# Kernel tuning notes

Measured on AMD Instinct MI355X. Metric: run time of the kernel, lower is better.

The kernel has to match this reference:

```python
import jax, jax.numpy as jnp
import numpy as np

BS, SL, D, NH = 2, 2048, 1024, 16
HD = D // NH
SCALE = D ** (-0.5)  # NOTE: source scales by full model dim, not head dim


def setup_inputs() -> dict:
    key = jax.random.key(0)
    k1, k2, k3 = jax.random.split(key, 3)
    return {
        "input_sequence": jax.random.normal(k1, (BS, SL, D), dtype=jnp.float32),
        "w_qkv": jax.random.normal(k2, (D, 3 * D), dtype=jnp.float32) * (D ** -0.5),
        "w_out": jax.random.normal(k3, (D, D), dtype=jnp.float32) * (D ** -0.5),
    }


def reference(input_sequence, w_qkv, w_out):
    bs, sl, od = input_sequence.shape
    nh, hd = NH, od // NH
    qkv = input_sequence @ w_qkv                      # [bs, sl, 3d]
    q, k, v = jnp.split(qkv, 3, axis=-1)              # each [bs, sl, d]
    q = q * SCALE

    def heads(x):  # [bs, sl, d] -> [bs, nh, sl, hd]
        return x.reshape(bs, sl, nh, hd).transpose(0, 2, 1, 3)

    q, k, v = heads(q), heads(k), heads(v)
    scores = jnp.einsum("bhqd,bhkd->bhqk", q, k)      # [bs, nh, sl, sl]
    weights = jax.nn.softmax(scores, axis=-1)
    ctx = jnp.einsum("bhqk,bhkd->bhqd", weights, v)   # [bs, nh, sl, hd]
    ctx = ctx.transpose(0, 2, 1, 3).reshape(bs, sl, od)
    return ctx @ w_out
```

## Files before the change

kernel.cpp:

```cpp
#include <hip/hip_runtime.h>
#include <cstdint>
#include <cstddef>

typedef float f32x4 __attribute__((ext_vector_type(4)));
typedef float f32x16 __attribute__((ext_vector_type(16)));
typedef __bf16 bf16x8 __attribute__((ext_vector_type(8)));
typedef __bf16 bf16x4 __attribute__((ext_vector_type(4)));
typedef uint32_t u32x4 __attribute__((ext_vector_type(4)));

static constexpr int BSZ = 2, SL = 2048, DM = 1024, NH = 16, HD = 64;
static constexpr int MROWS = BSZ * SL;
static constexpr float LOG2E = 1.4426950408889634f;
static constexpr float QSCALE = 0.03125f * LOG2E;

__device__ __forceinline__ f32x4 mfma16(bf16x8 a, bf16x8 b, f32x4 c) {
    return __builtin_amdgcn_mfma_f32_16x16x32_bf16(a, b, c, 0, 0, 0);
}
__device__ __forceinline__ f32x16 mfma32(bf16x8 a, bf16x8 b, f32x16 c) {
    return __builtin_amdgcn_mfma_f32_32x32x16_bf16(a, b, c, 0, 0, 0);
}
__device__ __forceinline__ uint32_t pkbf(float lo, float hi) {
    uint16_t a = __builtin_bit_cast(uint16_t, (__bf16)lo);
    uint16_t b = __builtin_bit_cast(uint16_t, (__bf16)hi);
    return ((uint32_t)b << 16) | (uint32_t)a;
}
__device__ __forceinline__ float fexp2(float x) {
#if __has_builtin(__builtin_amdgcn_exp2f)
    return __builtin_amdgcn_exp2f(x);
#else
    float r; asm volatile("v_exp_f32 %0, %1" : "=v"(r) : "v"(x)); return r;
#endif
}
__device__ __forceinline__ void gload16(const void* g, void* l) {
    __builtin_amdgcn_global_load_lds(
        (const __attribute__((address_space(1))) uint32_t*)g,
        (__attribute__((address_space(3))) uint32_t*)l, 16, 0, 0);
}

__global__ __launch_bounds__(256) void r19_cast(const float* __restrict__ in,
                                                __bf16* __restrict__ out, int n) {
    int i = (blockIdx.x * 256 + threadIdx.x) * 4;
    if (i >= n) return;
    float4 v = *(const float4*)&in[i];
    bf16x4 o;
    o.x = (__bf16)v.x; o.y = (__bf16)v.y; o.z = (__bf16)v.z; o.w = (__bf16)v.w;
    *(bf16x4*)&out[i] = o;
}

__global__ __launch_bounds__(256) void r19_transpose_cast(const float* __restrict__ in,
                                                          __bf16* __restrict__ out,
                                                          int R, int C) {
    __shared__ float tile[32][33];
    int c0 = blockIdx.x * 32, r0 = blockIdx.y * 32;
    int tx = threadIdx.x & 31, ty = threadIdx.x >> 5;
#pragma unroll
    for (int i = 0; i < 32; i += 8)
        tile[ty + i][tx] = in[(size_t)(r0 + ty + i) * C + c0 + tx];
    __syncthreads();
#pragma unroll
    for (int i = 0; i < 32; i += 8)
        out[(size_t)(c0 + ty + i) * R + r0 + tx] = (__bf16)tile[tx][ty + i];
}

__global__ __launch_bounds__(512, 1) void r19_gemm1(
    const __bf16* __restrict__ A, const __bf16* __restrict__ Bt,
    int M, int N, int K,
    __bf16* __restrict__ qb, __bf16* __restrict__ kb, __bf16* __restrict__ vtb)
{
    __shared__ __bf16 arena[65536];
    const int L  = blockIdx.x + 12 * blockIdx.y;
    const int Ls = (L & 7) * 24 + (L >> 3);
    const int bx = Ls % 12, by = Ls / 12;
    const int n0 = bx * 256, m0 = by * 256;

    const int tid  = threadIdx.x;
    const int wave = tid >> 6, lane = tid & 63;
    const int wr = wave >> 2, wc = wave & 3;
    const int lcol = lane & 15, lgrp = lane >> 4;

    const int srow = wave * 16 + (lane >> 3);
    const int slin = lane & 7;

    f32x4 acc[8][4] = {};
    const int NT = K / 64;

#pragma unroll
    for (int q = 0; q < 4; ++q) {
#pragma unroll
        for (int j = 0; j < 2; ++j) {
            const int r = srow + j * 8;
            const int slot = slin ^ (r & 7);
            const __bf16* src = (q < 2)
                ? &A [(size_t)(m0 + q * 128 + r) * K + slot * 8]
                : &Bt[(size_t)(n0 + (q - 2) * 128 + r) * K + slot * 8];
            gload16(src, &arena[(q < 2 ? q * 8192 : 16384 + (q - 2) * 8192)
                                + (wave * 2 + j) * 512]);
        }
    }
    asm volatile("s_waitcnt vmcnt(0)" ::: "memory");
    __builtin_amdgcn_s_barrier();
    __builtin_amdgcn_sched_barrier(0);

    for (int t = 0; t < NT; ++t) {
        const int cur = t & 1;
        const __bf16* Ab = &arena[cur * 32768];
        const __bf16* Bb = Ab + 16384;
        __bf16* dbuf = &arena[(cur ^ 1) * 32768];
        const int kn = (t + 1) * 64;
        const bool pf = (t + 1 < NT);

#pragma unroll
        for (int q = 0; q < 4; ++q) {
            const int mh = q >> 1, ksub = q & 1;
            if (pf) {
#pragma unroll
                for (int j = 0; j < 2; ++j) {
                    const int r = srow + j * 8;
                    const int slot = slin ^ (r & 7);
                    const __bf16* src = (q < 2)
                        ? &A [(size_t)(m0 + q * 128 + r) * K + kn + slot * 8]
                        : &Bt[(size_t)(n0 + (q - 2) * 128 + r) * K + kn + slot * 8];
                    gload16(src, dbuf + (q < 2 ? q * 8192 : 16384 + (q - 2) * 8192)
                                      + (wave * 2 + j) * 512);
                }
            }
            bf16x8 af[4], bfr[4];
#pragma unroll
            for (int f = 0; f < 4; ++f) {
                const int ra = wr * 128 + mh * 64 + f * 16 + lcol;
                const int ua = (ksub * 4 + lgrp) ^ (ra & 7);
                af[f] = *(const bf16x8*)&Ab[(ra & 127) * 64 + ua * 8 + (ra >> 7) * 8192];
                const int rb = wc * 64 + f * 16 + lcol;
                const int ub = (ksub * 4 + lgrp) ^ (rb & 7);
                bfr[f] = *(const bf16x8*)&Bb[(rb & 127) * 64 + ub * 8 + (rb >> 7) * 8192];
            }
            __builtin_amdgcn_s_setprio(1);
#pragma unroll
            for (int fm = 0; fm < 4; ++fm)
#pragma unroll
                for (int fn = 0; fn < 4; ++fn)
                    acc[mh * 4 + fm][fn] = mfma16(af[fm], bfr[fn], acc[mh * 4 + fm][fn]);
            __builtin_amdgcn_s_setprio(0);
        }
        asm volatile("s_waitcnt vmcnt(0)" ::: "memory");
        __builtin_amdgcn_s_barrier();
        __builtin_amdgcn_sched_barrier(0);
    }

#pragma unroll
    for (int fm = 0; fm < 8; ++fm) {
#pragma unroll
        for (int fn = 0; fn < 4; ++fn) {
            const int n = n0 + wc * 64 + fn * 16 + lcol;
            const int sec = n >> 10, nm = n & 1023;
            const int hh = nm >> 6, d = nm & 63;
#pragma unroll
            for (int r = 0; r < 4; ++r) {
                const int m = m0 + wr * 128 + fm * 16 + lgrp * 4 + r;
                const int b = m >> 11, s = m & 2047;
                const size_t bh = (size_t)(b * NH + hh);
                const float v = acc[fm][fn][r];
                if (sec == 0)      qb[(bh * SL + s) * HD + d]  = (__bf16)(v * QSCALE);
                else if (sec == 1) kb[(bh * SL + s) * HD + d]  = (__bf16)v;
                else               vtb[(bh * HD + d) * SL + s] = (__bf16)v;
            }
        }
    }
}

template <int BN>
__global__ __launch_bounds__(256) void r19_gemm2(
    const __bf16* __restrict__ A, const __bf16* __restrict__ Bt,
    float* __restrict__ ob, int M, int N, int K)
{
    constexpr int BM = 128, BK = 32;
    constexpr int FN = BN / 32;
    __shared__ __bf16 As[BM * BK];
    __shared__ __bf16 Bs[BN * BK];
    const int tid  = threadIdx.x;
    const int m0   = blockIdx.y * BM, n0 = blockIdx.x * BN;
    const int wave = tid >> 6, lane = tid & 63;
    const int lcol = lane & 15, lgrp = lane >> 4;
    const int wm   = (wave >> 1) * 64, wn = (wave & 1) * (BN / 2);
    const int grow = lane >> 2, gcol = (lane & 3) * 8;

    f32x4 acc[4][FN] = {};

    for (int k0 = 0; k0 < K; k0 += BK) {
        {
            const int cA0 = 2 * wave;
            gload16(&A[(size_t)(m0 + cA0 * 16 + grow) * K + k0 + gcol], &As[cA0 * 512]);
            gload16(&A[(size_t)(m0 + (cA0 + 1) * 16 + grow) * K + k0 + gcol], &As[(cA0 + 1) * 512]);
            if constexpr (BN == 128) {
                gload16(&Bt[(size_t)(n0 + cA0 * 16 + grow) * K + k0 + gcol], &Bs[cA0 * 512]);
                gload16(&Bt[(size_t)(n0 + (cA0 + 1) * 16 + grow) * K + k0 + gcol], &Bs[(cA0 + 1) * 512]);
            } else {
                gload16(&Bt[(size_t)(n0 + wave * 16 + grow) * K + k0 + gcol], &Bs[wave * 512]);
            }
        }
        __syncthreads();
        bf16x8 af[4], bfr[FN];
#pragma unroll
        for (int f = 0; f < 4; ++f)
            af[f] = *(const bf16x8*)&As[(wm + f * 16 + lcol) * BK + lgrp * 8];
#pragma unroll
        for (int f = 0; f < FN; ++f)
            bfr[f] = *(const bf16x8*)&Bs[(wn + f * 16 + lcol) * BK + lgrp * 8];
#pragma unroll
        for (int fm = 0; fm < 4; ++fm)
#pragma unroll
            for (int fn = 0; fn < FN; ++fn)
                acc[fm][fn] = mfma16(af[fm], bfr[fn], acc[fm][fn]);
        __syncthreads();
    }

#pragma unroll
    for (int fm = 0; fm < 4; ++fm)
#pragma unroll
        for (int fn = 0; fn < FN; ++fn) {
            int n = n0 + wn + fn * 16 + lcol;
#pragma unroll
            for (int r = 0; r < 4; ++r) {
                int m = m0 + wm + fm * 16 + lgrp * 4 + r;
                ob[(size_t)m * N + n] = acc[fm][fn][r];
            }
        }
}

#define PV_STEP(a0,a1,a2,a3,a4,a5,a6,a7, KS) do {                               \
    uint32_t w0 = pkbf(a0, a1), w1 = pkbf(a2, a3);                              \
    uint32_t w2 = pkbf(a4, a5), w3 = pkbf(a6, a7);                              \
    asm volatile("v_permlane32_swap_b32 %0, %1" : "+v"(w0), "+v"(w2));          \
    asm volatile("v_permlane32_swap_b32 %0, %1" : "+v"(w1), "+v"(w3));          \
    u32x4 pw = {w0, w1, w2, w3};                                                \
    bf16x8 pf = __builtin_bit_cast(bf16x8, pw);                                 \
    const int cv = (((KS) * 2 + h) ^ swz8) * 8;                                 \
    bf16x8 vf0 = *(const bf16x8*)&Vl[lq * 64 + cv];                             \
    bf16x8 vf1 = *(const bf16x8*)&Vl[(lq + 32) * 64 + cv];                      \
    accT0 = mfma32(vf0, pf, accT0);                                             \
    accT1 = mfma32(vf1, pf, accT1);                                             \
} while (0)

#define TILE_BODY(TI, KA, KB, VA, VB) do {                                      \
    const int cur = (TI) & 1;                                                   \
    {                                                                           \
        __bf16* dK = &arena[cur * 8192 + oA];                                   \
        __bf16* dV = dK + 4096;                                                 \
        *(int4*)dK = KA;  *(int4*)(dK + 2048) = KB;                             \
        *(int4*)dV = VA;  *(int4*)(dV + 2048) = VB;                             \
    }                                                                           \
    if ((TI) + 2 < NT) {                                                        \
        const __bf16* nK = KgA + (size_t)((TI) + 2) * 64 * HD;                  \
        const __bf16* nV = VgA + (size_t)((TI) + 2) * 64;                       \
        KA = *(const int4*)(nK);                                                \
        KB = *(const int4*)(nK + (size_t)32 * HD);                              \
        VA = *(const int4*)(nV);                                                \
        VB = *(const int4*)(nV + (size_t)32 * SL);                              \
    }                                                                           \
    asm volatile("s_waitcnt lgkmcnt(0)" ::: "memory");                          \
    __builtin_amdgcn_s_barrier();                                               \
    __builtin_amdgcn_sched_barrier(0);                                          \
    const __bf16* Kl = &arena[cur * 8192];                                      \
    const __bf16* Vl = Kl + 4096;                                               \
    f32x16 s0 = {}, s1 = {};                                                    \
    __builtin_amdgcn_s_setprio(1);                                              \
    _Pragma("unroll")                                                           \
    for (int t4 = 0; t4 < 4; ++t4) {                                            \
        const int cv = ((t4 * 2 + h) ^ swz8) * 8;                               \
        bf16x8 kf0 = *(const bf16x8*)&Kl[lq * 64 + cv];                         \
        bf16x8 kf1 = *(const bf16x8*)&Kl[(lq + 32) * 64 + cv];                  \
        s0 = mfma32(kf0, qf[t4], s0);                                           \
        s1 = mfma32(kf1, qf[t4], s1);                                           \
    }                                                                           \
    __builtin_amdgcn_s_setprio(0);                                              \
    float p0[16], p1[16];                                                       \
    _Pragma("unroll")                                                           \
    for (int i = 0; i < 16; ++i) { p0[i] = fexp2(s0[i]); p1[i] = fexp2(s1[i]); }\
    __builtin_amdgcn_s_setprio(1);                                              \
    PV_STEP(p0[0], p0[1], p0[2], p0[3], p0[4], p0[5], p0[6], p0[7], 0);         \
    PV_STEP(p0[8], p0[9], p0[10], p0[11], p0[12], p0[13], p0[14], p0[15], 1);   \
    PV_STEP(p1[0], p1[1], p1[2], p1[3], p1[4], p1[5], p1[6], p1[7], 2);         \
    PV_STEP(p1[8], p1[9], p1[10], p1[11], p1[12], p1[13], p1[14], p1[15], 3);   \
    __builtin_amdgcn_s_setprio(0);                                              \
    float a16[16];                                                              \
    _Pragma("unroll")                                                           \
    for (int i = 0; i < 16; ++i) a16[i] = p0[i] + p1[i];                        \
    _Pragma("unroll")                                                           \
    for (int i = 0; i < 8; ++i) a16[i] += a16[i + 8];                           \
    _Pragma("unroll")                                                           \
    for (int i = 0; i < 4; ++i) a16[i] += a16[i + 4];                           \
    float lt = (a16[0] + a16[1]) + (a16[2] + a16[3]);                           \
    lt += __shfl_xor(lt, 32);                                                   \
    l_run += lt;                                                                \
} while (0)

__global__ __launch_bounds__(256) void r19_attn(
    const __bf16* __restrict__ qb, const __bf16* __restrict__ kb,
    const __bf16* __restrict__ vtb, __bf16* __restrict__ ctx)
{
    __shared__ __bf16 arena[16384];
    const int L = blockIdx.x + 16 * blockIdx.y;
    const int xcd = L & 7, j = L >> 3;
    const int bh = xcd * 4 + (j & 3);
    const int qblk = j >> 2;
    const int tid  = threadIdx.x;
    const int wave = tid >> 6, lane = tid & 63;
    const int lq = lane & 31, h = lane >> 5;
    const int swz8 = lq & 7;
    const int q0 = qblk * 128 + wave * 32;

    const __bf16* Q  = qb  + ((size_t)bh * SL + q0) * HD;
    const __bf16* Kg = kb  + (size_t)bh * SL * HD;
    const __bf16* Vg = vtb + (size_t)bh * HD * SL;

    const int rA = tid >> 3, cA = tid & 7;
    const int sA = cA ^ (rA & 7);
    const int oA = rA * 64 + sA * 8;

    bf16x8 qf[4];
#pragma unroll
    for (int t = 0; t < 4; ++t)
        qf[t] = *(const bf16x8*)&Q[(size_t)lq * HD + t * 16 + h * 8];

    f32x16 accT0 = {}, accT1 = {};
    float l_run = 0.f;

    const __bf16* KgA = Kg + (size_t)rA * HD + cA * 8;
    const __bf16* VgA = Vg + (size_t)rA * SL + cA * 8;
    int4 kA0 = *(const int4*)(KgA);
    int4 kB0 = *(const int4*)(KgA + (size_t)32 * HD);
    int4 vA0 = *(const int4*)(VgA);
    int4 vB0 = *(const int4*)(VgA + (size_t)32 * SL);
    int4 kA1 = *(const int4*)(KgA + (size_t)64 * HD);
    int4 kB1 = *(const int4*)(KgA + (size_t)96 * HD);
    int4 vA1 = *(const int4*)(VgA + 64);
    int4 vB1 = *(const int4*)(VgA + (size_t)32 * SL + 64);

    constexpr int NT = SL / 64;
    for (int t = 0; t < NT; t += 2) {
        TILE_BODY(t,     kA0, kB0, vA0, vB0);
        TILE_BODY(t + 1, kA1, kB1, vA1, vB1);
    }

    float inv = 1.f / l_run;
    __syncthreads();
    __bf16* Osw = &arena[wave * 2304];
#pragma unroll
    for (int r = 0; r < 16; ++r) {
        int d0 = (r & 3) + 8 * (r >> 2) + 4 * h;
        Osw[lq * 72 + d0]      = (__bf16)(accT0[r] * inv);
        Osw[lq * 72 + 32 + d0] = (__bf16)(accT1[r] * inv);
    }
    asm volatile("s_waitcnt lgkmcnt(0)" ::: "memory");
    __builtin_amdgcn_sched_barrier(0);
    const int b = bh >> 4, head = bh & 15;
    const int qr = lane >> 1, seg = (lane & 1) * 32;
    __bf16* dst = &ctx[((size_t)b * SL + q0 + qr) * DM + head * HD + seg];
#pragma unroll
    for (int c = 0; c < 4; ++c)
        *(bf16x8*)&dst[c * 8] = *(const bf16x8*)&Osw[qr * 72 + seg + c * 8];
}

extern "C" void kernel_launch(void* const* d_in, const int* in_sizes, int n_in,
                              void* d_out, int out_size, void* d_ws, size_t ws_size,
                              hipStream_t stream) {
    const float* x    = (const float*)d_in[0];
    const float* wqkv = (const float*)d_in[1];
    const float* wout = (const float*)d_in[2];
    float* out = (float*)d_out;

    __bf16* ws    = (__bf16*)d_ws;
    __bf16* xb    = ws;
    __bf16* wqkvT = xb    + (size_t)MROWS * DM;
    __bf16* woutT = wqkvT + (size_t)3 * DM * DM;
    __bf16* qbuf  = woutT + (size_t)DM * DM;
    __bf16* kbuf  = qbuf  + (size_t)MROWS * DM;
    __bf16* vtbuf = kbuf  + (size_t)MROWS * DM;
    __bf16* ctxb  = vtbuf + (size_t)MROWS * DM;

    r19_cast<<<dim3((MROWS * DM) / 1024), dim3(256), 0, stream>>>(x, xb, MROWS * DM);
    r19_transpose_cast<<<dim3(96, 32), dim3(256), 0, stream>>>(wqkv, wqkvT, DM, 3 * DM);
    r19_transpose_cast<<<dim3(32, 32), dim3(256), 0, stream>>>(wout, woutT, DM, DM);

    r19_gemm1<<<dim3(12, 16), dim3(512), 0, stream>>>(
        xb, wqkvT, MROWS, 3 * DM, DM, qbuf, kbuf, vtbuf);

    r19_attn<<<dim3(16, 32), dim3(256), 0, stream>>>(qbuf, kbuf, vtbuf, ctxb);

    r19_gemm2<64><<<dim3(16, 32), dim3(256), 0, stream>>>(
        ctxb, woutT, out, MROWS, DM, DM);
}
```

Measured before the change: 142.3 us.

## Restructure QKV GEMM main loop with stage-ahead prefetch and per-phase barriers

The QKV projection GEMM loop now issues the whole next k-tile prefetch at the top of each iteration. It waits with vmcnt(8), so only the current tile must have landed while the next stays in flight, instead of draining all loads at the end of the iteration. The four compute phases are reordered k-sub-major so B fragments are loaded from LDS once and reused for both M halves, which cuts LDS reads. Each phase is bracketed with extra workgroup barriers and an lgkmcnt wait to keep the waves in lockstep around the MFMA bursts. These added barriers cost synchronisation and may offset the gains. Kernels are also renamed from r19 to r20.

After: 147.0 us. 1.03x slower.

```diff
diff --git a/kernel.cpp b/kernel.cpp
--- a/kernel.cpp
+++ b/kernel.cpp
@@ -37,7 +37,7 @@
         (__attribute__((address_space(3))) uint32_t*)l, 16, 0, 0);
 }
 
-__global__ __launch_bounds__(256) void r19_cast(const float* __restrict__ in,
+__global__ __launch_bounds__(256) void r20_cast(const float* __restrict__ in,
                                                 __bf16* __restrict__ out, int n) {
     int i = (blockIdx.x * 256 + threadIdx.x) * 4;
     if (i >= n) return;
@@ -47,7 +47,7 @@
     *(bf16x4*)&out[i] = o;
 }
 
-__global__ __launch_bounds__(256) void r19_transpose_cast(const float* __restrict__ in,
+__global__ __launch_bounds__(256) void r20_transpose_cast(const float* __restrict__ in,
                                                           __bf16* __restrict__ out,
                                                           int R, int C) {
     __shared__ float tile[32][33];
@@ -62,7 +62,7 @@
         out[(size_t)(c0 + ty + i) * R + r0 + tx] = (__bf16)tile[tx][ty + i];
 }
 
-__global__ __launch_bounds__(512, 1) void r19_gemm1(
+__global__ __launch_bounds__(512, 1) void r20_gemm1(
     const __bf16* __restrict__ A, const __bf16* __restrict__ Bt,
     int M, int N, int K,
     __bf16* __restrict__ qb, __bf16* __restrict__ kb, __bf16* __restrict__ vtb)
@@ -84,56 +84,62 @@
     f32x4 acc[8][4] = {};
     const int NT = K / 64;
 
-#pragma unroll
-    for (int q = 0; q < 4; ++q) {
-#pragma unroll
-        for (int j = 0; j < 2; ++j) {
-            const int r = srow + j * 8;
-            const int slot = slin ^ (r & 7);
-            const __bf16* src = (q < 2)
-                ? &A [(size_t)(m0 + q * 128 + r) * K + slot * 8]
-                : &Bt[(size_t)(n0 + (q - 2) * 128 + r) * K + slot * 8];
-            gload16(src, &arena[(q < 2 ? q * 8192 : 16384 + (q - 2) * 8192)
-                                + (wave * 2 + j) * 512]);
-        }
-    }
-    asm volatile("s_waitcnt vmcnt(0)" ::: "memory");
-    __builtin_amdgcn_s_barrier();
-    __builtin_amdgcn_sched_barrier(0);
+#define R20_STAGE(TI, BUFP) do {                                                \
+        const int kk_ = (TI) * 64;                                              \
+        _Pragma("unroll")                                                       \
+        for (int q_ = 0; q_ < 4; ++q_) {                                        \
+            _Pragma("unroll")                                                   \
+            for (int j_ = 0; j_ < 2; ++j_) {                                    \
+                const int r_ = srow + j_ * 8;                                   \
+                const int slot_ = slin ^ (r_ & 7);                              \
+                const __bf16* src_ = (q_ < 2)                                   \
+                    ? &A [(size_t)(m0 + q_ * 128 + r_) * K + kk_ + slot_ * 8]   \
+                    : &Bt[(size_t)(n0 + (q_ - 2) * 128 + r_) * K + kk_ + slot_ * 8]; \
+                gload16(src_, (BUFP) + (q_ < 2 ? q_ * 8192                      \
+                                               : 16384 + (q_ - 2) * 8192)       \
+                              + (wave * 2 + j_) * 512);                         \
+            }                                                                   \
+        }                                                                       \
+    } while (0)
+
+    R20_STAGE(0, &arena[0]);
 
     for (int t = 0; t < NT; ++t) {
         const int cur = t & 1;
         const __bf16* Ab = &arena[cur * 32768];
         const __bf16* Bb = Ab + 16384;
-        __bf16* dbuf = &arena[(cur ^ 1) * 32768];
-        const int kn = (t + 1) * 64;
-        const bool pf = (t + 1 < NT);
-
-#pragma unroll
-        for (int q = 0; q < 4; ++q) {
-            const int mh = q >> 1, ksub = q & 1;
-            if (pf) {
-#pragma unroll
-                for (int j = 0; j < 2; ++j) {
-                    const int r = srow + j * 8;
-                    const int slot = slin ^ (r & 7);
-                    const __bf16* src = (q < 2)
-                        ? &A [(size_t)(m0 + q * 128 + r) * K + kn + slot * 8]
-                        : &Bt[(size_t)(n0 + (q - 2) * 128 + r) * K + kn + slot * 8];
-                    gload16(src, dbuf + (q < 2 ? q * 8192 : 16384 + (q - 2) * 8192)
-                                      + (wave * 2 + j) * 512);
+
+        if (t + 1 < NT) {
+            R20_STAGE(t + 1, &arena[(cur ^ 1) * 32768]);
+            asm volatile("s_waitcnt vmcnt(8)" ::: "memory");
+        } else {
+            asm volatile("s_waitcnt vmcnt(0)" ::: "memory");
+        }
+        __builtin_amdgcn_s_barrier();
+        __builtin_amdgcn_sched_barrier(0);
+
+        bf16x8 bfr[4];
+#pragma unroll
+        for (int ph = 0; ph < 4; ++ph) {
+            const int ksub = ph >> 1, mh = ph & 1;
+            if (mh == 0) {
+#pragma unroll
+                for (int f = 0; f < 4; ++f) {
+                    const int rb = wc * 64 + f * 16 + lcol;
+                    const int ub = (ksub * 4 + lgrp) ^ (rb & 7);
+                    bfr[f] = *(const bf16x8*)&Bb[(rb & 127) * 64 + ub * 8 + (rb >> 7) * 8192];
                 }
             }
-            bf16x8 af[4], bfr[4];
+            bf16x8 af[4];
 #pragma unroll
             for (int f = 0; f < 4; ++f) {
                 const int ra = wr * 128 + mh * 64 + f * 16 + lcol;
                 const int ua = (ksub * 4 + lgrp) ^ (ra & 7);
                 af[f] = *(const bf16x8*)&Ab[(ra & 127) * 64 + ua * 8 + (ra >> 7) * 8192];
-                const int rb = wc * 64 + f * 16 + lcol;
-                const int ub = (ksub * 4 + lgrp) ^ (rb & 7);
-                bfr[f] = *(const bf16x8*)&Bb[(rb & 127) * 64 + ub * 8 + (rb >> 7) * 8192];
-            }
+            }
+            __builtin_amdgcn_s_barrier();
+            asm volatile("s_waitcnt lgkmcnt(0)" ::: "memory");
+            __builtin_amdgcn_sched_barrier(0);
             __builtin_amdgcn_s_setprio(1);
 #pragma unroll
             for (int fm = 0; fm < 4; ++fm)
@@ -141,11 +147,10 @@
                 for (int fn = 0; fn < 4; ++fn)
                     acc[mh * 4 + fm][fn] = mfma16(af[fm], bfr[fn], acc[mh * 4 + fm][fn]);
             __builtin_amdgcn_s_setprio(0);
-        }
-        asm volatile("s_waitcnt vmcnt(0)" ::: "memory");
-        __builtin_amdgcn_s_barrier();
-        __builtin_amdgcn_sched_barrier(0);
-    }
+            __builtin_amdgcn_s_barrier();
+        }
+    }
+#undef R20_STAGE
 
 #pragma unroll
     for (int fm = 0; fm < 8; ++fm) {
@@ -169,7 +174,7 @@
 }
 
 template <int BN>
-__global__ __launch_bounds__(256) void r19_gemm2(
+__global__ __launch_bounds__(256) void r20_gemm2(
     const __bf16* __restrict__ A, const __bf16* __restrict__ Bt,
     float* __restrict__ ob, int M, int N, int K)
 {
@@ -294,7 +299,7 @@
     l_run += lt;                                                                \
 } while (0)
 
-__global__ __launch_bounds__(256) void r19_attn(
+__global__ __launch_bounds__(256) void r20_attn(
     const __bf16* __restrict__ qb, const __bf16* __restrict__ kb,
     const __bf16* __restrict__ vtb, __bf16* __restrict__ ctx)
 {
@@ -378,15 +383,15 @@
     __bf16* vtbuf = kbuf  + (size_t)MROWS * DM;
     __bf16* ctxb  = vtbuf + (size_t)MROWS * DM;
 
-    r19_cast<<<dim3((MROWS * DM) / 1024), dim3(256), 0, stream>>>(x, xb, MROWS * DM);
-    r19_transpose_cast<<<dim3(96, 32), dim3(256), 0, stream>>>(wqkv, wqkvT, DM, 3 * DM);
-    r19_transpose_cast<<<dim3(32, 32), dim3(256), 0, stream>>>(wout, woutT, DM, DM);
-
-    r19_gemm1<<<dim3(12, 16), dim3(512), 0, stream>>>(
+    r20_cast<<<dim3((MROWS * DM) / 1024), dim3(256), 0, stream>>>(x, xb, MROWS * DM);
+    r20_transpose_cast<<<dim3(96, 32), dim3(256), 0, stream>>>(wqkv, wqkvT, DM, 3 * DM);
+    r20_transpose_cast<<<dim3(32, 32), dim3(256), 0, stream>>>(wout, woutT, DM, DM);
+
+    r20_gemm1<<<dim3(12, 16), dim3(512), 0, stream>>>(
         xb, wqkvT, MROWS, 3 * DM, DM, qbuf, kbuf, vtbuf);
 
-    r19_attn<<<dim3(16, 32), dim3(256), 0, stream>>>(qbuf, kbuf, vtbuf, ctxb);
-
-    r19_gemm2<64><<<dim3(16, 32), dim3(256), 0, stream>>>(
+    r20_attn<<<dim3(16, 32), dim3(256), 0, stream>>>(qbuf, kbuf, vtbuf, ctxb);
+
+    r20_gemm2<64><<<dim3(16, 32), dim3(256), 0, stream>>>(
         ctxb, woutT, out, MROWS, DM, DM);
 }
```
